# Performance work log

Hardware: AMD Instinct MI355X
Metric: run time of the kernel (lower is better)

## Reference

```python
import jax, jax.numpy as jnp
import numpy as np

ALPHA = 8.3  # depth-similarity sharpness from the Depth-aware CNN paper
KH = KW = 3
PAD = 1


def _extract_patches(t, kh, kw, pad):
    # t: [B, C, H, W] -> [B, C, kh*kw, H, W] (stride 1, zero pad)
    B, C, H, W = t.shape
    tp = jnp.pad(t, ((0, 0), (0, 0), (pad, pad), (pad, pad)))
    views = [tp[:, :, i:i + H, j:j + W] for i in range(kh) for j in range(kw)]
    return jnp.stack(views, axis=2)


def setup_inputs() -> dict:
    key = jax.random.key(0)
    k1, k2, k3 = jax.random.split(key, 3)
    B, Cin, H, W = 4, 32, 256, 256
    Cout = 32
    x = jax.random.normal(k1, (B, Cin, H, W), dtype=jnp.float32)
    depth = jax.random.uniform(k2, (B, 1, H, W), dtype=jnp.float32)
    stdv = 1.0 / np.sqrt(Cin * KH * KW)
    weight = jax.random.uniform(k3, (Cout, Cin, KH, KW), dtype=jnp.float32,
                                minval=-stdv, maxval=stdv)
    return {"x": x, "depth": depth, "weight": weight}


def reference(x, depth, weight):
    # Depth-aware convolution: each sampled input value is modulated by
    # exp(-ALPHA * |D(center) - D(neighbor)|) before the conv accumulation.
    B, C, H, W = x.shape
    O = weight.shape[0]
    x_pat = _extract_patches(x, KH, KW, PAD)          # [B, C, 9, H, W]
    d_pat = _extract_patches(depth, KH, KW, PAD)      # [B, 1, 9, H, W]
    d_center = depth[:, :, None, :, :]                # [B, 1, 1, H, W]
    sim = jnp.exp(-ALPHA * jnp.abs(d_center - d_pat))  # [B, 1, 9, H, W]
    w = weight.reshape(O, C, KH * KW)                 # [O, C, 9]
    out = jnp.einsum('bckhw,ock->bohw', x_pat * sim, w)
    return out
```

## Files before the change

### kernel.cpp

```cpp
#include <hip/hip_runtime.h>
#include <hip/hip_bf16.h>
#include <math.h>


#define ALPHA_F 8.3f

constexpr int B_    = 4;
constexpr int CIN   = 32;
constexpr int COUT  = 32;
constexpr int H_    = 256;
constexpr int W_    = 256;
constexpr int KTAPS = 9;
constexpr int HW    = H_ * W_;

typedef __attribute__((ext_vector_type(8))) short bf16x8;
typedef __attribute__((ext_vector_type(4))) float f32x4;

static __device__ __forceinline__ short f2bf(float f) {
    __hip_bfloat16 h = __float2bfloat16(f);
    return __builtin_bit_cast(short, h);
}

__global__ void prep_wfrag(const float* __restrict__ w, short* __restrict__ wf) {
    int idx = blockIdx.x * 256 + threadIdx.x;
    if (idx >= KTAPS * 2 * 64 * 8) return;
    int e  = idx & 7;
    int l  = (idx >> 3) & 63;
    int t  = (idx >> 9) & 1;
    int ij = idx >> 10;
    int o  = t * 16 + (l & 15);
    int c  = (l >> 4) * 8 + e;
    wf[idx] = f2bf(w[(o * CIN + c) * KTAPS + ij]);
}

__global__ __launch_bounds__(256, 4)
void dconv_fused9(const float* __restrict__ x,
                  const float* __restrict__ depth,
                  const short* __restrict__ wf,
                  float* __restrict__ out) {
    __shared__ __align__(16) short xs[6][66][40];
    __shared__ float dsh[6][66];

    const int bid  = (int)blockIdx.x;
    const int bswz = (bid & 7) * 128 + (bid >> 3);

    const int b    = bswz >> 8;
    const int hseg = (bswz >> 2) & 63;
    const int wseg = (bswz & 3) << 6;
    const int h0   = hseg << 2;
    const int tid  = threadIdx.x;
    const int lane = tid & 63;
    const float* xb  = x + (size_t)b * CIN * HW;
    const float* dpl = depth + (size_t)b * HW;

    float xv0[24], xv1[24];
#pragma unroll
    for (int it = 0; it < 24; ++it) {
        const int idx = it * 256 + tid;
        const int q   = idx & 63;
        const int cp  = (idx >> 6) & 15;
        const int r   = idx >> 10;
        const int row = h0 + r - 1;
        const int rowc = ((unsigned)row < (unsigned)H_) ? row : h0;
        const size_t gb = (size_t)(2 * cp) * HW + rowc * W_ + wseg + q;
        xv0[it] = xb[gb];
        xv1[it] = xb[gb + HW];
    }
    float hv0, hv1;
    {
        const int side = tid & 1;
        const int hrc  = tid >> 1;
        const int hcp  = hrc & 15;
        const int hr   = (hrc >> 4) % 6;
        const int hrow = h0 + hr - 1;
        const int hwx  = wseg - 1 + side * 65;
        const bool hok = (tid < 192) &&
                         ((unsigned)hrow < (unsigned)H_) &&
                         ((unsigned)hwx  < (unsigned)W_);
        const size_t gb = (size_t)(2 * hcp) * HW +
                          (hok ? (size_t)(hrow * W_ + hwx) : 0);
        hv0 = xb[gb];
        hv1 = xb[gb + HW];
    }
    float dv0, dv1;
    {
        const int r0   = tid / 66;
        const int q0   = tid - r0 * 66;
        const int row0 = h0 + r0 - 1;
        const int wx0  = wseg - 1 + q0;
        const bool ok0 = ((unsigned)row0 < (unsigned)H_) &&
                         ((unsigned)wx0  < (unsigned)W_);
        dv0 = dpl[ok0 ? (row0 * W_ + wx0) : 0];

        const int k1   = tid + 256;
        const int r1   = (k1 / 66) % 6;
        const int q1   = k1 - (k1 / 66) * 66;
        const int row1 = h0 + r1 - 1;
        const int wx1  = wseg - 1 + q1;
        const bool ok1 = (k1 < 396) &&
                         ((unsigned)row1 < (unsigned)H_) &&
                         ((unsigned)wx1  < (unsigned)W_);
        dv1 = dpl[ok1 ? (row1 * W_ + wx1) : 0];
    }

#pragma unroll
    for (int it = 0; it < 24; ++it) {
        const int idx = it * 256 + tid;
        const int q   = idx & 63;
        const int cp  = (idx >> 6) & 15;
        const int r   = idx >> 10;
        const bool ok = ((unsigned)(h0 + r - 1) < (unsigned)H_);
        const float f0 = ok ? xv0[it] : 0.f;
        const float f1 = ok ? xv1[it] : 0.f;
        const int v = (int)(unsigned short)f2bf(f0) |
                      ((int)(unsigned short)f2bf(f1) << 16);
        ((int*)&xs[r][q + 1][0])[cp] = v;
    }
    if (tid < 192) {
        const int side = tid & 1;
        const int hrc  = tid >> 1;
        const int hcp  = hrc & 15;
        const int hr   = hrc >> 4;
        const int hrow = h0 + hr - 1;
        const int hwx  = wseg - 1 + side * 65;
        const bool hok = ((unsigned)hrow < (unsigned)H_) &&
                         ((unsigned)hwx  < (unsigned)W_);
        const float f0 = hok ? hv0 : 0.f;
        const float f1 = hok ? hv1 : 0.f;
        const int v = (int)(unsigned short)f2bf(f0) |
                      ((int)(unsigned short)f2bf(f1) << 16);
        ((int*)&xs[hr][side * 65][0])[hcp] = v;
    }
    {
        const int r0   = tid / 66;
        const int q0   = tid - r0 * 66;
        const bool ok0 = ((unsigned)(h0 + r0 - 1) < (unsigned)H_) &&
                         ((unsigned)(wseg - 1 + q0) < (unsigned)W_);
        dsh[r0][q0] = ok0 ? dv0 : 0.f;
        const int k1 = tid + 256;
        if (k1 < 396) {
            const int r1   = k1 / 66;
            const int q1   = k1 - r1 * 66;
            const bool ok1 = ((unsigned)(h0 + r1 - 1) < (unsigned)H_) &&
                             ((unsigned)(wseg - 1 + q1) < (unsigned)W_);
            dsh[r1][q1] = ok1 ? dv1 : 0.f;
        }
    }

    const bf16x8* wfv = (const bf16x8*)wf;
    bf16x8 wa[2 * KTAPS];
#pragma unroll
    for (int k = 0; k < 2 * KTAPS; ++k) wa[k] = wfv[k * 64 + lane];

    __syncthreads();

    const int w    = tid >> 6;
    const int n    = lane & 15;
    const int cg   = (lane >> 4) * 8;
    const int rl   = w + 1;
    const int hrow = h0 + w;
    const int orow = (lane >> 4) * 4;
    const f32x4 z = {0.f, 0.f, 0.f, 0.f};

#pragma unroll
    for (int sub = 0; sub < 4; ++sub) {
        const int pl = sub * 16 + n + 1;
        const int wp = wseg + sub * 16 + n;
        const float dc = dsh[rl][pl];

        float s[KTAPS];
#pragma unroll
        for (int ij = 0; ij < KTAPS; ++ij) {
            const int di = ij / 3 - 1;
            const int dj = ij % 3 - 1;
            const bool ok = ((unsigned)(hrow + di) < (unsigned)H_) &&
                            ((unsigned)(wp + dj) < (unsigned)W_);
            s[ij] = ok ? __expf(-ALPHA_F * fabsf(dc - dsh[rl + di][pl + dj])) : 0.f;
        }

        f32x4 acc0 = z, acc1 = z;
#pragma unroll
        for (int ij = 0; ij < KTAPS; ++ij) {
            const int di = ij / 3 - 1;
            const int dj = ij % 3 - 1;
            const bf16x8 bfrag = *(const bf16x8*)&xs[rl + di][pl + dj][cg];
            const f32x4 t0 = __builtin_amdgcn_mfma_f32_16x16x32_bf16(wa[ij * 2 + 0], bfrag, z, 0, 0, 0);
            const f32x4 t1 = __builtin_amdgcn_mfma_f32_16x16x32_bf16(wa[ij * 2 + 1], bfrag, z, 0, 0, 0);
#pragma unroll
            for (int j = 0; j < 4; ++j) {
                acc0[j] = fmaf(s[ij], t0[j], acc0[j]);
                acc1[j] = fmaf(s[ij], t1[j], acc1[j]);
            }
        }

        float* ob = out + (size_t)b * COUT * HW + hrow * W_ + wp;
#pragma unroll
        for (int j = 0; j < 4; ++j) {
            __builtin_nontemporal_store(acc0[j], ob + (size_t)(orow + j) * HW);
            __builtin_nontemporal_store(acc1[j], ob + (size_t)(orow + j + 16) * HW);
        }
    }
}

__global__ __launch_bounds__(256)
void dconv_fallback(const float* __restrict__ x,
                    const float* __restrict__ depth,
                    const float* __restrict__ wgt,
                    float* __restrict__ out) {
    const int w  = threadIdx.x;
    const int bh = blockIdx.x;
    const int b  = bh >> 8;
    const int h  = bh & 255;

    const float* dplane = depth + (size_t)b * HW;
    const float  dc     = dplane[h * W_ + w];

    float acc[COUT];
#pragma unroll
    for (int o = 0; o < COUT; ++o) acc[o] = 0.f;

    const float* xb = x + (size_t)b * CIN * HW;

    for (int i = 0; i < 3; ++i) {
        const int  hh  = h + i - 1;
        const bool okh = ((unsigned)hh < (unsigned)H_);
        for (int j = 0; j < 3; ++j) {
            const int  ww = w + j - 1;
            const bool ok = okh && ((unsigned)ww < (unsigned)W_);
            const int  ij = i * 3 + j;
            const float dpv = ok ? dplane[hh * W_ + ww] : 0.f;
            const float sv  = __expf(-ALPHA_F * fabsf(dc - dpv));
            const int base = hh * W_ + ww;
#pragma unroll
            for (int c = 0; c < CIN; ++c) {
                const float v = (ok ? xb[c * HW + base] : 0.f) * sv;
#pragma unroll
                for (int o = 0; o < COUT; ++o) {
                    acc[o] = fmaf(v, wgt[(o * CIN + c) * KTAPS + ij], acc[o]);
                }
            }
        }
    }

    float* ob = out + ((size_t)b * COUT * H_ + h) * W_ + w;
#pragma unroll
    for (int o = 0; o < COUT; ++o) ob[o * HW] = acc[o];
}

extern "C" void kernel_launch(void* const* d_in, const int* in_sizes, int n_in,
                              void* d_out, int out_size, void* d_ws, size_t ws_size,
                              hipStream_t stream) {
    const float* x     = (const float*)d_in[0];
    const float* depth = (const float*)d_in[1];
    const float* wgt   = (const float*)d_in[2];
    float*       out   = (float*)d_out;

    const size_t wf_bytes = (size_t)(KTAPS * 2 * 64 * 8) * sizeof(short);

    if (ws_size >= wf_bytes) {
        short* wf = (short*)d_ws;
        prep_wfrag<<<(KTAPS * 2 * 64 * 8 + 255) / 256, 256, 0, stream>>>(wgt, wf);
        dconv_fused9<<<1024, 256, 0, stream>>>(x, depth, wf, out);
    } else {
        dconv_fallback<<<B_ * H_, 256, 0, stream>>>(x, depth, wgt, out);
    }
}
```

Measured before the change: 24.12 us.

## Process eight rows per block with register-prefetched second half overlapping compute

```diff
diff --git a/kernel.cpp b/kernel.cpp
--- a/kernel.cpp
+++ b/kernel.cpp
@@ -33,21 +33,21 @@
     wf[idx] = f2bf(w[(o * CIN + c) * KTAPS + ij]);
 }
 
-__global__ __launch_bounds__(256, 4)
-void dconv_fused9(const float* __restrict__ x,
-                  const float* __restrict__ depth,
-                  const short* __restrict__ wf,
-                  float* __restrict__ out) {
-    __shared__ __align__(16) short xs[6][66][40];
-    __shared__ float dsh[6][66];
+__global__ __launch_bounds__(256, 2)
+void dconv_fused10(const float* __restrict__ x,
+                   const float* __restrict__ depth,
+                   const short* __restrict__ wf,
+                   float* __restrict__ out) {
+    __shared__ __align__(16) short xs[10][66][40];
+    __shared__ float dsh[10][66];
 
     const int bid  = (int)blockIdx.x;
-    const int bswz = (bid & 7) * 128 + (bid >> 3);
-
-    const int b    = bswz >> 8;
-    const int hseg = (bswz >> 2) & 63;
+    const int bswz = (bid & 7) * 64 + (bid >> 3);
+
+    const int b    = bswz >> 7;
+    const int hseg = (bswz >> 2) & 31;
     const int wseg = (bswz & 3) << 6;
-    const int h0   = hseg << 2;
+    const int h0   = hseg << 3;
     const int tid  = threadIdx.x;
     const int lane = tid & 63;
     const float* xb  = x + (size_t)b * CIN * HW;
@@ -132,15 +132,15 @@
         ((int*)&xs[hr][side * 65][0])[hcp] = v;
     }
     {
-        const int r0   = tid / 66;
-        const int q0   = tid - r0 * 66;
+        const int r0 = tid / 66;
+        const int q0 = tid - r0 * 66;
         const bool ok0 = ((unsigned)(h0 + r0 - 1) < (unsigned)H_) &&
                          ((unsigned)(wseg - 1 + q0) < (unsigned)W_);
         dsh[r0][q0] = ok0 ? dv0 : 0.f;
         const int k1 = tid + 256;
         if (k1 < 396) {
-            const int r1   = k1 / 66;
-            const int q1   = k1 - r1 * 66;
+            const int r1 = k1 / 66;
+            const int q1 = k1 - r1 * 66;
             const bool ok1 = ((unsigned)(h0 + r1 - 1) < (unsigned)H_) &&
                              ((unsigned)(wseg - 1 + q1) < (unsigned)W_);
             dsh[r1][q1] = ok1 ? dv1 : 0.f;
@@ -152,52 +152,194 @@
 #pragma unroll
     for (int k = 0; k < 2 * KTAPS; ++k) wa[k] = wfv[k * 64 + lane];
 
+    float yv0[16], yv1[16];
+#pragma unroll
+    for (int it = 0; it < 16; ++it) {
+        const int idx = it * 256 + tid;
+        const int q   = idx & 63;
+        const int cp  = (idx >> 6) & 15;
+        const int r2  = idx >> 10;
+        const int row = h0 + 5 + r2;
+        const int rowc = ((unsigned)row < (unsigned)H_) ? row : h0;
+        const size_t gb = (size_t)(2 * cp) * HW + rowc * W_ + wseg + q;
+        yv0[it] = xb[gb];
+        yv1[it] = xb[gb + HW];
+    }
+    float hw0, hw1;
+    {
+        const int side = tid & 1;
+        const int hrc  = tid >> 1;
+        const int hcp  = hrc & 15;
+        const int hr2  = (hrc >> 4) & 3;
+        const int hrow = h0 + 5 + hr2;
+        const int hwx  = wseg - 1 + side * 65;
+        const bool hok = (tid < 128) &&
+                         ((unsigned)hrow < (unsigned)H_) &&
+                         ((unsigned)hwx  < (unsigned)W_);
+        const size_t gb = (size_t)(2 * hcp) * HW +
+                          (hok ? (size_t)(hrow * W_ + hwx) : 0);
+        hw0 = xb[gb];
+        hw1 = xb[gb + HW];
+    }
+    float dw0, dw1;
+    {
+        const int r0   = tid / 66;
+        const int q0   = tid - r0 * 66;
+        const int row0 = h0 + 5 + r0;
+        const int wx0  = wseg - 1 + q0;
+        const bool ok0 = ((unsigned)row0 < (unsigned)H_) &&
+                         ((unsigned)wx0  < (unsigned)W_);
+        dw0 = dpl[ok0 ? (row0 * W_ + wx0) : 0];
+
+        const int k1   = tid + 256;
+        const int q1   = k1 - 198;
+        const int r1   = (k1 / 66) & 3;
+        const int q1b  = k1 - (k1 / 66) * 66;
+        const int row1 = h0 + 5 + r1;
+        const int wx1  = wseg - 1 + q1b;
+        const bool ok1 = (k1 < 264) &&
+                         ((unsigned)row1 < (unsigned)H_) &&
+                         ((unsigned)wx1  < (unsigned)W_);
+        (void)q1;
+        dw1 = dpl[ok1 ? (row1 * W_ + wx1) : 0];
+    }
+
     __syncthreads();
 
     const int w    = tid >> 6;
     const int n    = lane & 15;
     const int cg   = (lane >> 4) * 8;
-    const int rl   = w + 1;
-    const int hrow = h0 + w;
     const int orow = (lane >> 4) * 4;
     const f32x4 z = {0.f, 0.f, 0.f, 0.f};
 
-#pragma unroll
-    for (int sub = 0; sub < 4; ++sub) {
-        const int pl = sub * 16 + n + 1;
-        const int wp = wseg + sub * 16 + n;
-        const float dc = dsh[rl][pl];
-
-        float s[KTAPS];
-#pragma unroll
-        for (int ij = 0; ij < KTAPS; ++ij) {
-            const int di = ij / 3 - 1;
-            const int dj = ij % 3 - 1;
-            const bool ok = ((unsigned)(hrow + di) < (unsigned)H_) &&
-                            ((unsigned)(wp + dj) < (unsigned)W_);
-            s[ij] = ok ? __expf(-ALPHA_F * fabsf(dc - dsh[rl + di][pl + dj])) : 0.f;
+    {
+        const int rl   = w + 1;
+        const int hrow = h0 + w;
+#pragma unroll
+        for (int sub = 0; sub < 4; ++sub) {
+            const int pl = sub * 16 + n + 1;
+            const int wp = wseg + sub * 16 + n;
+            const float dc = dsh[rl][pl];
+
+            float s[KTAPS];
+#pragma unroll
+            for (int ij = 0; ij < KTAPS; ++ij) {
+                const int di = ij / 3 - 1;
+                const int dj = ij % 3 - 1;
+                const bool ok = ((unsigned)(hrow + di) < (unsigned)H_) &&
+                                ((unsigned)(wp + dj) < (unsigned)W_);
+                s[ij] = ok ? __expf(-ALPHA_F * fabsf(dc - dsh[rl + di][pl + dj])) : 0.f;
+            }
+
+            f32x4 acc0 = z, acc1 = z;
+#pragma unroll
+            for (int ij = 0; ij < KTAPS; ++ij) {
+                const int di = ij / 3 - 1;
+                const int dj = ij % 3 - 1;
+                const bf16x8 bfrag = *(const bf16x8*)&xs[rl + di][pl + dj][cg];
+                const f32x4 t0 = __builtin_amdgcn_mfma_f32_16x16x32_bf16(wa[ij * 2 + 0], bfrag, z, 0, 0, 0);
+                const f32x4 t1 = __builtin_amdgcn_mfma_f32_16x16x32_bf16(wa[ij * 2 + 1], bfrag, z, 0, 0, 0);
+#pragma unroll
+                for (int j = 0; j < 4; ++j) {
+                    acc0[j] = fmaf(s[ij], t0[j], acc0[j]);
+                    acc1[j] = fmaf(s[ij], t1[j], acc1[j]);
+                }
+            }
+
+            float* ob = out + (size_t)b * COUT * HW + hrow * W_ + wp;
+#pragma unroll
+            for (int j = 0; j < 4; ++j) {
+                __builtin_nontemporal_store(acc0[j], ob + (size_t)(orow + j) * HW);
+                __builtin_nontemporal_store(acc1[j], ob + (size_t)(orow + j + 16) * HW);
+            }
         }
-
-        f32x4 acc0 = z, acc1 = z;
-#pragma unroll
-        for (int ij = 0; ij < KTAPS; ++ij) {
-            const int di = ij / 3 - 1;
-            const int dj = ij % 3 - 1;
-            const bf16x8 bfrag = *(const bf16x8*)&xs[rl + di][pl + dj][cg];
-            const f32x4 t0 = __builtin_amdgcn_mfma_f32_16x16x32_bf16(wa[ij * 2 + 0], bfrag, z, 0, 0, 0);
-            const f32x4 t1 = __builtin_amdgcn_mfma_f32_16x16x32_bf16(wa[ij * 2 + 1], bfrag, z, 0, 0, 0);
+    }
+
+#pragma unroll
+    for (int it = 0; it < 16; ++it) {
+        const int idx = it * 256 + tid;
+        const int q   = idx & 63;
+        const int cp  = (idx >> 6) & 15;
+        const int r2  = idx >> 10;
+        const bool ok = ((unsigned)(h0 + 5 + r2) < (unsigned)H_);
+        const float f0 = ok ? yv0[it] : 0.f;
+        const float f1 = ok ? yv1[it] : 0.f;
+        const int v = (int)(unsigned short)f2bf(f0) |
+                      ((int)(unsigned short)f2bf(f1) << 16);
+        ((int*)&xs[6 + r2][q + 1][0])[cp] = v;
+    }
+    if (tid < 128) {
+        const int side = tid & 1;
+        const int hrc  = tid >> 1;
+        const int hcp  = hrc & 15;
+        const int hr2  = hrc >> 4;
+        const int hrow = h0 + 5 + hr2;
+        const int hwx  = wseg - 1 + side * 65;
+        const bool hok = ((unsigned)hrow < (unsigned)H_) &&
+                         ((unsigned)hwx  < (unsigned)W_);
+        const float f0 = hok ? hw0 : 0.f;
+        const float f1 = hok ? hw1 : 0.f;
+        const int v = (int)(unsigned short)f2bf(f0) |
+                      ((int)(unsigned short)f2bf(f1) << 16);
+        ((int*)&xs[6 + hr2][side * 65][0])[hcp] = v;
+    }
+    {
+        const int r0 = tid / 66;
+        const int q0 = tid - r0 * 66;
+        const bool ok0 = ((unsigned)(h0 + 5 + r0) < (unsigned)H_) &&
+                         ((unsigned)(wseg - 1 + q0) < (unsigned)W_);
+        dsh[6 + r0][q0] = ok0 ? dw0 : 0.f;
+        const int k1 = tid + 256;
+        if (k1 < 264) {
+            const int r1 = k1 / 66;
+            const int q1 = k1 - r1 * 66;
+            const bool ok1 = ((unsigned)(h0 + 5 + r1) < (unsigned)H_) &&
+                             ((unsigned)(wseg - 1 + q1) < (unsigned)W_);
+            dsh[6 + r1][q1] = ok1 ? dw1 : 0.f;
+        }
+    }
+    __syncthreads();
+
+    {
+        const int rl   = w + 5;
+        const int hrow = h0 + 4 + w;
+#pragma unroll
+        for (int sub = 0; sub < 4; ++sub) {
+            const int pl = sub * 16 + n + 1;
+            const int wp = wseg + sub * 16 + n;
+            const float dc = dsh[rl][pl];
+
+            float s[KTAPS];
+#pragma unroll
+            for (int ij = 0; ij < KTAPS; ++ij) {
+                const int di = ij / 3 - 1;
+                const int dj = ij % 3 - 1;
+                const bool ok = ((unsigned)(hrow + di) < (unsigned)H_) &&
+                                ((unsigned)(wp + dj) < (unsigned)W_);
+                s[ij] = ok ? __expf(-ALPHA_F * fabsf(dc - dsh[rl + di][pl + dj])) : 0.f;
+            }
+
+            f32x4 acc0 = z, acc1 = z;
+#pragma unroll
+            for (int ij = 0; ij < KTAPS; ++ij) {
+                const int di = ij / 3 - 1;
+                const int dj = ij % 3 - 1;
+                const bf16x8 bfrag = *(const bf16x8*)&xs[rl + di][pl + dj][cg];
+                const f32x4 t0 = __builtin_amdgcn_mfma_f32_16x16x32_bf16(wa[ij * 2 + 0], bfrag, z, 0, 0, 0);
+                const f32x4 t1 = __builtin_amdgcn_mfma_f32_16x16x32_bf16(wa[ij * 2 + 1], bfrag, z, 0, 0, 0);
+#pragma unroll
+                for (int j = 0; j < 4; ++j) {
+                    acc0[j] = fmaf(s[ij], t0[j], acc0[j]);
+                    acc1[j] = fmaf(s[ij], t1[j], acc1[j]);
+                }
+            }
+
+            float* ob = out + (size_t)b * COUT * HW + hrow * W_ + wp;
 #pragma unroll
             for (int j = 0; j < 4; ++j) {
-                acc0[j] = fmaf(s[ij], t0[j], acc0[j]);
-                acc1[j] = fmaf(s[ij], t1[j], acc1[j]);
-            }
-        }
-
-        float* ob = out + (size_t)b * COUT * HW + hrow * W_ + wp;
-#pragma unroll
-        for (int j = 0; j < 4; ++j) {
-            __builtin_nontemporal_store(acc0[j], ob + (size_t)(orow + j) * HW);
-            __builtin_nontemporal_store(acc1[j], ob + (size_t)(orow + j + 16) * HW);
+                __builtin_nontemporal_store(acc0[j], ob + (size_t)(orow + j) * HW);
+                __builtin_nontemporal_store(acc1[j], ob + (size_t)(orow + j + 16) * HW);
+            }
         }
     }
 }
@@ -260,7 +402,7 @@
     if (ws_size >= wf_bytes) {
         short* wf = (short*)d_ws;
         prep_wfrag<<<(KTAPS * 2 * 64 * 8 + 255) / 256, 256, 0, stream>>>(wgt, wf);
-        dconv_fused9<<<1024, 256, 0, stream>>>(x, depth, wf, out);
+        dconv_fused10<<<512, 256, 0, stream>>>(x, depth, wf, out);
     } else {
         dconv_fallback<<<B_ * H_, 256, 0, stream>>>(x, depth, wgt, out);
     }
```

Result: slower. 24.63 us (+2.1%).
